# Kernel tuning notes

Measured on AMD Instinct MI355X. Metric: run time of the kernel, lower is better.

The kernel has to match this reference:

```python
import jax, jax.numpy as jnp
import numpy as np
from jax import lax

E = 3  # num_experts

def _maxpool2(x):
    return lax.reduce_window(x, -jnp.inf, lax.max, (1, 1, 2, 2), (1, 1, 2, 2), 'VALID')

def _mixed_conv(x, experts, routing, stride, pad):
    # per-sample expert-mixed convolution via grouped conv trick
    B, Ci, H, W = x.shape
    _, Co, _, k, _ = experts.shape
    kern = jnp.einsum('be,eoikl->boikl', routing, experts).reshape(B * Co, Ci, k, k)
    y = lax.conv_general_dilated(
        x.reshape(1, B * Ci, H, W), kern, (stride, stride),
        [(pad, pad), (pad, pad)],
        dimension_numbers=('NCHW', 'OIHW', 'NCHW'),
        feature_group_count=B)
    return y.reshape(B, Co, y.shape[2], y.shape[3])

def _dyres_conv(x, experts, rw, rb, stride=1, pad=1):
    # DyRes mode 'A': routing from avg-pool + spatial-std descriptors, softmax over experts
    avg = x.mean((2, 3))
    std = x.std((2, 3))
    r = jax.nn.softmax((avg + std) @ rw.T + rb, axis=-1)  # [B, E]
    return _mixed_conv(x, experts, r, stride, pad)

def _cond_conv(x, experts, rw, rb, stride=1, pad=1):
    # CondConv: sigmoid routing from global average pool
    r = jax.nn.sigmoid(x.mean((2, 3)) @ rw.T + rb)  # [B, E]
    return _mixed_conv(x, experts, r, stride, pad)

def _conv_init(key, co, ci, k):
    return jax.random.normal(key, (E, co, ci, k, k), jnp.float32) * np.sqrt(2.0 / (ci * k * k)).astype(np.float32)

def setup_inputs() -> dict:
    key = jax.random.key(0)
    ks = jax.random.split(key, 20)
    B = 512
    d = {}
    d['x'] = jax.random.normal(ks[0], (B, 3, 32, 32), jnp.float32)
    d['dw1'] = _conv_init(ks[1], 64, 3, 3)
    d['rw1'] = jax.random.normal(ks[2], (E, 3), jnp.float32) * 0.1
    d['rb1'] = jnp.zeros((E,), jnp.float32)
    d['dw2'] = _conv_init(ks[3], 192, 64, 3)
    d['rw2'] = jax.random.normal(ks[4], (E, 64), jnp.float32) * 0.1
    d['rb2'] = jnp.zeros((E,), jnp.float32)
    d['dw3'] = _conv_init(ks[5], 384, 192, 3)
    d['rw3'] = jax.random.normal(ks[6], (E, 192), jnp.float32) * 0.1
    d['rb3'] = jnp.zeros((E,), jnp.float32)
    d['cw4'] = _conv_init(ks[7], 256, 384, 3)
    d['cr4w'] = jax.random.normal(ks[8], (E, 384), jnp.float32) * 0.1
    d['cr4b'] = jnp.zeros((E,), jnp.float32)
    d['cw5'] = _conv_init(ks[9], 256, 256, 3)
    d['cr5w'] = jax.random.normal(ks[10], (E, 256), jnp.float32) * 0.1
    d['cr5b'] = jnp.zeros((E,), jnp.float32)
    d['fw1'] = jax.random.normal(ks[11], (4096, 1024), jnp.float32) * np.sqrt(2.0 / 1024).astype(np.float32)
    d['fb1'] = jnp.zeros((4096,), jnp.float32)
    d['fw2'] = jax.random.normal(ks[12], (4096, 4096), jnp.float32) * np.sqrt(2.0 / 4096).astype(np.float32)
    d['fb2'] = jnp.zeros((4096,), jnp.float32)
    d['fw3'] = jax.random.normal(ks[13], (100, 4096), jnp.float32) * np.sqrt(1.0 / 4096).astype(np.float32)
    d['fb3'] = jnp.zeros((100,), jnp.float32)
    return d

def reference(x, dw1, rw1, rb1, dw2, rw2, rb2, dw3, rw3, rb3,
              cw4, cr4w, cr4b, cw5, cr5w, cr5b,
              fw1, fb1, fw2, fb2, fw3, fb3):
    h = jax.nn.relu(_dyres_conv(x, dw1, rw1, rb1, stride=2))   # [B,64,16,16]
    h = _maxpool2(h)                                           # [B,64,8,8]
    h = jax.nn.relu(_dyres_conv(h, dw2, rw2, rb2))             # [B,192,8,8]
    h = _maxpool2(h)                                           # [B,192,4,4]
    h = jax.nn.relu(_dyres_conv(h, dw3, rw3, rb3))             # [B,384,4,4]
    h = jax.nn.relu(_cond_conv(h, cw4, cr4w, cr4b))            # [B,256,4,4]
    h = jax.nn.relu(_cond_conv(h, cw5, cr5w, cr5b))            # [B,256,4,4]
    h = _maxpool2(h)                                           # [B,256,2,2]
    h = h.reshape(h.shape[0], -1)                              # [B,1024]
    h = jax.nn.relu(h @ fw1.T + fb1)
    h = jax.nn.relu(h @ fw2.T + fb2)
    return h @ fw3.T + fb3                                     # [B,100]
```

## Files before the change

kernel.cpp:

```cpp
#include <hip/hip_runtime.h>
#include <math.h>


typedef unsigned short u16;
typedef unsigned int u32;
typedef short bf16x8 __attribute__((ext_vector_type(8)));
typedef float f32x4 __attribute__((ext_vector_type(4)));

__device__ __forceinline__ u16 bf16_rne(float f) {
    u32 u = __float_as_uint(f);
    return (u16)((u + 0x7fffu + ((u >> 16) & 1u)) >> 16);
}
__device__ __forceinline__ u32 packsplit(float v) {
    u16 h = bf16_rne(v);
    float hf = __uint_as_float((u32)h << 16);
    u16 l = bf16_rne(v - hf);
    return ((u32)h << 16) | l;
}
__device__ __forceinline__ float unpackf(u32 p) {
    return __uint_as_float(p & 0xffff0000u) + __uint_as_float(p << 16);
}
__device__ __forceinline__ int xcd_swz(int bid, int n) {
    if ((n & 7) != 0) return bid;
    int cpx = n >> 3;
    return (bid & 7) * cpx + (bid >> 3);
}

__global__ __launch_bounds__(256)
void wsplit_kernel(const float* __restrict__ W, u16* __restrict__ whi,
                   u16* __restrict__ wlo, int total, int Kper, int Kpad)
{
    int idx = blockIdx.x * 256 + threadIdx.x;
    if (idx >= total) return;
    int r = idx / Kpad, k = idx - r * Kpad;
    float v = (k < Kper) ? W[(size_t)r * Kper + k] : 0.f;
    u16 h = bf16_rne(v);
    whi[idx] = h;
    wlo[idx] = bf16_rne(v - __uint_as_float((u32)h << 16));
}

__global__ __launch_bounds__(256)
void wsplit_cl_kernel(const float* __restrict__ W, u16* __restrict__ whi,
                      u16* __restrict__ wlo, int total, int Ci)
{
    int idx = blockIdx.x * 256 + threadIdx.x;
    if (idx >= total) return;
    int Kper = 9 * Ci;
    int r = idx / Kper, kp = idx - r * Kper;
    int cell = kp / Ci, ci = kp - cell * Ci;
    float v = W[(size_t)r * Kper + ci * 9 + cell];
    u16 h = bf16_rne(v);
    whi[idx] = h;
    wlo[idx] = bf16_rne(v - __uint_as_float((u32)h << 16));
}

__global__ __launch_bounds__(64)
void stats_kernel(const float* __restrict__ actv, float* __restrict__ s,
                  int C, int HW, int use_std)
{
    int idx = blockIdx.x;
    size_t base = (size_t)idx * HW;
    int lane = threadIdx.x;
    float sum = 0.f, sq = 0.f;
    const float* p = actv + base;
    for (int i = lane; i < HW; i += 64) { float v = p[i]; sum += v; sq += v * v; }
#pragma unroll
    for (int off = 32; off > 0; off >>= 1) {
        sum += __shfl_down(sum, off);
        sq  += __shfl_down(sq, off);
    }
    if (lane == 0) {
        float inv = 1.f / (float)HW;
        float mean = sum * inv;
        float var = sq * inv - mean * mean;
        float outv = mean;
        if (use_std) outv += sqrtf(fmaxf(var, 0.f));
        s[idx] = outv;
    }
}

__global__ __launch_bounds__(384)
void stats_cl_kernel(const u32* __restrict__ act, float* __restrict__ s,
                     int H2, int W2, int C, int use_std)
{
    int b = blockIdx.x, c = threadIdx.x;
    int Hin = H2 - 2, Win = W2 - 2;
    float sum = 0.f, sq = 0.f;
    for (int h = 0; h < Hin; ++h)
        for (int w = 0; w < Win; ++w) {
            float v = unpackf(act[(((size_t)b * H2 + h + 1) * W2 + w + 1) * C + c]);
            sum += v; sq += v * v;
        }
    float inv = 1.f / (float)(Hin * Win);
    float mean = sum * inv;
    float var = sq * inv - mean * mean;
    float outv = mean;
    if (use_std) outv += sqrtf(fmaxf(var, 0.f));
    s[b * C + c] = outv;
}

__global__ __launch_bounds__(64)
void routing_kernel(const float* __restrict__ s, const float* __restrict__ rw,
                    const float* __restrict__ rb, float* __restrict__ r,
                    int C, int softmax_mode)
{
    int b = blockIdx.x;
    int lane = threadIdx.x;
    float d0 = 0.f, d1 = 0.f, d2 = 0.f;
    for (int c = lane; c < C; c += 64) {
        float sv = s[b * C + c];
        d0 += sv * rw[c];
        d1 += sv * rw[C + c];
        d2 += sv * rw[2 * C + c];
    }
#pragma unroll
    for (int off = 32; off > 0; off >>= 1) {
        d0 += __shfl_down(d0, off);
        d1 += __shfl_down(d1, off);
        d2 += __shfl_down(d2, off);
    }
    if (lane == 0) {
        d0 += rb[0]; d1 += rb[1]; d2 += rb[2];
        if (softmax_mode) {
            float mx = fmaxf(d0, fmaxf(d1, d2));
            float e0 = expf(d0 - mx), e1 = expf(d1 - mx), e2 = expf(d2 - mx);
            float inv = 1.f / (e0 + e1 + e2);
            r[b * 3 + 0] = e0 * inv;
            r[b * 3 + 1] = e1 * inv;
            r[b * 3 + 2] = e2 * inv;
        } else {
            r[b * 3 + 0] = 1.f / (1.f + expf(-d0));
            r[b * 3 + 1] = 1.f / (1.f + expf(-d1));
            r[b * 3 + 2] = 1.f / (1.f + expf(-d2));
        }
    }
}

template<int CI, int H2, int W2, int LGS, int LGOW>
__global__ __launch_bounds__(256, 2)
void cgemm_cl_kernel(const u16* __restrict__ Whi, const u16* __restrict__ Wlo,
                     const u32* __restrict__ Bpk, const float* __restrict__ rptr,
                     float* __restrict__ Cout, int M, int N, int Kper, int Kchunk)
{
    __shared__ __align__(16) u16 Ah[2][128 * 40], Al[2][128 * 40];
    __shared__ __align__(16) u16 Bh[2][128 * 40], Bl[2][128 * 40];
    const int tid = threadIdx.x;
    const int bx = xcd_swz(blockIdx.x, gridDim.x);
    const int n0 = bx << 7, m0 = blockIdx.y << 7;
    const int kq0 = blockIdx.z * Kchunk;

    const int rowA = tid >> 1, kh16 = (tid & 1) << 4;
    const int nB = tid & 127, kOff = (tid >> 7) << 4;

    const int nn = n0 + nB;
    const int bB = nn >> LGS;
    const int sidx = nn & ((1 << LGS) - 1);
    const int oh = sidx >> LGOW, ow = sidx & ((1 << LGOW) - 1);
    const long nBase = ((long)(bB * H2 + oh) * W2 + ow) * CI;

    const int lane = tid & 63, wv = tid >> 6;
    const int lm = lane & 15, qd = lane >> 4;
    const int wm = (wv & 1) << 6, wn = (wv >> 1) << 6;

    float rsv[3][4];
#pragma unroll
    for (int ni = 0; ni < 4; ++ni) {
        int n = n0 + wn + ni * 16 + lm;
        int b = n >> LGS;
#pragma unroll
        for (int e = 0; e < 3; ++e) rsv[e][ni] = rptr[b * 3 + e];
    }

    f32x4 acc[4][4], accS[4][4];
#pragma unroll
    for (int i = 0; i < 4; ++i)
#pragma unroll
        for (int j = 0; j < 4; ++j) {
            acc[i][j]  = (f32x4){0.f, 0.f, 0.f, 0.f};
            accS[i][j] = (f32x4){0.f, 0.f, 0.f, 0.f};
        }

    const int mg = m0 + rowA;
    const int nkz = Kchunk >> 5;
    const int NS = 3 * nkz;

    int eL = 0, kL = kq0;
    uint4 pA0, pA1, pA2, pA3;
    uint4 pQ0, pQ1, pQ2, pQ3;

    auto LOAD = [&]() {
        size_t aOff = ((size_t)(eL * M + mg)) * Kper + kL + kh16;
        const u16* hp = Whi + aOff;
        const u16* lp = Wlo + aOff;
        pA0 = *(const uint4*)hp; pA1 = *(const uint4*)(hp + 8);
        pA2 = *(const uint4*)lp; pA3 = *(const uint4*)(lp + 8);
        int k = kL + kOff;
        int cell = k / CI;
        int ci0 = k - cell * CI;
        int kh = (cell * 11) >> 5;
        int kw = cell - kh * 3;
        const u32* bp = Bpk + (nBase + (long)((kh * W2 + kw) * CI + ci0));
        pQ0 = *(const uint4*)bp;
        pQ1 = *(const uint4*)(bp + 4);
        pQ2 = *(const uint4*)(bp + 8);
        pQ3 = *(const uint4*)(bp + 12);
    };
    auto ADV = [&]() {
        kL += 32;
        if (kL == kq0 + Kchunk) { kL = kq0; ++eL; }
    };
    auto STORE = [&](int buf) {
        *(uint4*)(&Ah[buf][rowA * 40 + kh16])     = pA0;
        *(uint4*)(&Ah[buf][rowA * 40 + kh16 + 8]) = pA1;
        *(uint4*)(&Al[buf][rowA * 40 + kh16])     = pA2;
        *(uint4*)(&Al[buf][rowA * 40 + kh16 + 8]) = pA3;
        u32 qv[16] = {pQ0.x, pQ0.y, pQ0.z, pQ0.w, pQ1.x, pQ1.y, pQ1.z, pQ1.w,
                      pQ2.x, pQ2.y, pQ2.z, pQ2.w, pQ3.x, pQ3.y, pQ3.z, pQ3.w};
        u32 hw[8], lw[8];
#pragma unroll
        for (int j = 0; j < 8; ++j) {
            u32 p0 = qv[2 * j], p1 = qv[2 * j + 1];
            hw[j] = (p0 >> 16) | (p1 & 0xffff0000u);
            lw[j] = (p0 & 0xffffu) | (p1 << 16);
        }
        *(uint4*)(&Bh[buf][nB * 40 + kOff])     = make_uint4(hw[0], hw[1], hw[2], hw[3]);
        *(uint4*)(&Bh[buf][nB * 40 + kOff + 8]) = make_uint4(hw[4], hw[5], hw[6], hw[7]);
        *(uint4*)(&Bl[buf][nB * 40 + kOff])     = make_uint4(lw[0], lw[1], lw[2], lw[3]);
        *(uint4*)(&Bl[buf][nB * 40 + kOff + 8]) = make_uint4(lw[4], lw[5], lw[6], lw[7]);
    };
    auto COMPUTE = [&](int buf) {
        bf16x8 ah[4], al[4];
#pragma unroll
        for (int mi = 0; mi < 4; ++mi) {
            int row = wm + mi * 16 + lm;
            ah[mi] = *(const bf16x8*)(&Ah[buf][row * 40 + qd * 8]);
            al[mi] = *(const bf16x8*)(&Al[buf][row * 40 + qd * 8]);
        }
        __builtin_amdgcn_s_setprio(1);
#pragma unroll
        for (int ni = 0; ni < 4; ++ni) {
            int row = wn + ni * 16 + lm;
            bf16x8 bh = *(const bf16x8*)(&Bh[buf][row * 40 + qd * 8]);
            bf16x8 bl = *(const bf16x8*)(&Bl[buf][row * 40 + qd * 8]);
#pragma unroll
            for (int mi = 0; mi < 4; ++mi) {
                f32x4 c = acc[mi][ni];
                c = __builtin_amdgcn_mfma_f32_16x16x32_bf16(al[mi], bh, c, 0, 0, 0);
                c = __builtin_amdgcn_mfma_f32_16x16x32_bf16(ah[mi], bl, c, 0, 0, 0);
                c = __builtin_amdgcn_mfma_f32_16x16x32_bf16(ah[mi], bh, c, 0, 0, 0);
                acc[mi][ni] = c;
            }
        }
        __builtin_amdgcn_s_setprio(0);
    };

    LOAD(); ADV();
    int s = 0, buf = 0;
#pragma unroll
    for (int e = 0; e < 3; ++e) {
        for (int t = 0; t < nkz; ++t) {
            STORE(buf);
            if (s + 1 < NS) { LOAD(); ADV(); }
            asm volatile("s_waitcnt lgkmcnt(0)\n\ts_barrier" ::: "memory");
            COMPUTE(buf);
            buf ^= 1; ++s;
        }
#pragma unroll
        for (int mi = 0; mi < 4; ++mi)
#pragma unroll
            for (int ni = 0; ni < 4; ++ni) {
                accS[mi][ni] += acc[mi][ni] * rsv[e][ni];
                acc[mi][ni] = (f32x4){0.f, 0.f, 0.f, 0.f};
            }
    }

    const bool atom = (gridDim.z > 1);
#pragma unroll
    for (int ni = 0; ni < 4; ++ni) {
        int n = n0 + wn + ni * 16 + lm;
#pragma unroll
        for (int mi = 0; mi < 4; ++mi)
#pragma unroll
            for (int r = 0; r < 4; ++r) {
                int m = m0 + wm + mi * 16 + qd * 4 + r;
                if (m >= M) continue;
                float v = accS[mi][ni][r];
                if (atom) atomicAdd(&Cout[(size_t)n * M + m], v);
                else      Cout[(size_t)n * M + m] = v;
            }
    }
}

__global__ __launch_bounds__(256, 2)
void cgemm_l1_kernel(const u16* __restrict__ Whi, const u16* __restrict__ Wlo,
                     const u32* __restrict__ Bpk, const float* __restrict__ rptr,
                     float* __restrict__ Cout, int M, int N)
{
    __shared__ __align__(16) u16 Ah[2][128 * 40], Al[2][128 * 40];
    __shared__ __align__(16) u16 Bh[2][128 * 40], Bl[2][128 * 40];
    const int tid = threadIdx.x;
    const int bx = xcd_swz(blockIdx.x, gridDim.x);
    const int n0 = bx << 7;
    const int Kper = 27, Kpad = 32;
    const int H = 32, W = 32;

    const int rowA = tid >> 1, kh16 = (tid & 1) << 4;
    const int nB = tid & 127, kOff = (tid >> 7) << 4;

    const int nn = n0 + nB;
    const int bB = nn >> 8;
    const int sidx = nn & 255;
    const int ohs = (sidx >> 4) * 2 - 1;
    const int ows = (sidx & 15) * 2 - 1;
    const long nBase = (long)bB * 3072 + (long)ohs * W + ows;

    const int lane = tid & 63, wv = tid >> 6;
    const int lm = lane & 15, qd = lane >> 4;
    const int wm = (wv & 1) << 6, wn = (wv >> 1) << 6;

    float rsv[3][4];
#pragma unroll
    for (int ni = 0; ni < 4; ++ni) {
        int n = n0 + wn + ni * 16 + lm;
        int b = n >> 8;
#pragma unroll
        for (int e = 0; e < 3; ++e) rsv[e][ni] = rptr[b * 3 + e];
    }

    f32x4 acc[4][4], accS[4][4];
#pragma unroll
    for (int i = 0; i < 4; ++i)
#pragma unroll
        for (int j = 0; j < 4; ++j) {
            acc[i][j]  = (f32x4){0.f, 0.f, 0.f, 0.f};
            accS[i][j] = (f32x4){0.f, 0.f, 0.f, 0.f};
        }

    const int mg = rowA;
    int eL = 0;
    uint4 pA0, pA1, pA2, pA3;
    u32 pB[16];

    auto LOAD = [&]() {
        size_t aOff = ((size_t)(eL * M + mg)) * Kpad + kh16;
        const u16* hp = Whi + aOff;
        const u16* lp = Wlo + aOff;
        pA0 = *(const uint4*)hp; pA1 = *(const uint4*)(hp + 8);
        pA2 = *(const uint4*)lp; pA3 = *(const uint4*)(lp + 8);
#pragma unroll
        for (int j = 0; j < 16; ++j) {
            int k = kOff + j;
            int ci = (int)((unsigned)k / 9u);
            int r9 = k - ci * 9;
            int kh = (int)(((unsigned)r9 * 11u) >> 5);
            int kw = r9 - kh * 3;
            int ih = ohs + kh, iw = ows + kw;
            u32 p = 0;
            if (k < Kper && (unsigned)ih < (unsigned)H && (unsigned)iw < (unsigned)W)
                p = Bpk[nBase + (long)ci * 1024 + kh * W + kw];
            pB[j] = p;
        }
    };
    auto STORE = [&](int buf) {
        *(uint4*)(&Ah[buf][rowA * 40 + kh16])     = pA0;
        *(uint4*)(&Ah[buf][rowA * 40 + kh16 + 8]) = pA1;
        *(uint4*)(&Al[buf][rowA * 40 + kh16])     = pA2;
        *(uint4*)(&Al[buf][rowA * 40 + kh16 + 8]) = pA3;
        u32 hw[8], lw[8];
#pragma unroll
        for (int j = 0; j < 8; ++j) {
            u32 p0 = pB[2 * j], p1 = pB[2 * j + 1];
            hw[j] = (p0 >> 16) | (p1 & 0xffff0000u);
            lw[j] = (p0 & 0xffffu) | (p1 << 16);
        }
        *(uint4*)(&Bh[buf][nB * 40 + kOff])     = make_uint4(hw[0], hw[1], hw[2], hw[3]);
        *(uint4*)(&Bh[buf][nB * 40 + kOff + 8]) = make_uint4(hw[4], hw[5], hw[6], hw[7]);
        *(uint4*)(&Bl[buf][nB * 40 + kOff])     = make_uint4(lw[0], lw[1], lw[2], lw[3]);
        *(uint4*)(&Bl[buf][nB * 40 + kOff + 8]) = make_uint4(lw[4], lw[5], lw[6], lw[7]);
    };
    auto COMPUTE = [&](int buf) {
        bf16x8 ah[4], al[4];
#pragma unroll
        for (int mi = 0; mi < 4; ++mi) {
            int row = wm + mi * 16 + lm;
            ah[mi] = *(const bf16x8*)(&Ah[buf][row * 40 + qd * 8]);
            al[mi] = *(const bf16x8*)(&Al[buf][row * 40 + qd * 8]);
        }
        __builtin_amdgcn_s_setprio(1);
#pragma unroll
        for (int ni = 0; ni < 4; ++ni) {
            int row = wn + ni * 16 + lm;
            bf16x8 bh = *(const bf16x8*)(&Bh[buf][row * 40 + qd * 8]);
            bf16x8 bl = *(const bf16x8*)(&Bl[buf][row * 40 + qd * 8]);
#pragma unroll
            for (int mi = 0; mi < 4; ++mi) {
                f32x4 c = acc[mi][ni];
                c = __builtin_amdgcn_mfma_f32_16x16x32_bf16(al[mi], bh, c, 0, 0, 0);
                c = __builtin_amdgcn_mfma_f32_16x16x32_bf16(ah[mi], bl, c, 0, 0, 0);
                c = __builtin_amdgcn_mfma_f32_16x16x32_bf16(ah[mi], bh, c, 0, 0, 0);
                acc[mi][ni] = c;
            }
        }
        __builtin_amdgcn_s_setprio(0);
    };

    LOAD(); ++eL;
    int buf = 0;
#pragma unroll
    for (int e = 0; e < 3; ++e) {
        STORE(buf);
        if (e < 2) { LOAD(); ++eL; }
        asm volatile("s_waitcnt lgkmcnt(0)\n\ts_barrier" ::: "memory");
        COMPUTE(buf);
        buf ^= 1;
#pragma unroll
        for (int mi = 0; mi < 4; ++mi)
#pragma unroll
            for (int ni = 0; ni < 4; ++ni) {
                accS[mi][ni] += acc[mi][ni] * rsv[e][ni];
                acc[mi][ni] = (f32x4){0.f, 0.f, 0.f, 0.f};
            }
    }

#pragma unroll
    for (int ni = 0; ni < 4; ++ni) {
        int n = n0 + wn + ni * 16 + lm;
#pragma unroll
        for (int mi = 0; mi < 4; ++mi)
#pragma unroll
            for (int r = 0; r < 4; ++r) {
                int m = wm + mi * 16 + qd * 4 + r;
                if (m >= M) continue;
                Cout[(size_t)n * M + m] = accS[mi][ni][r];
            }
    }
}

template<int BIAS, int TROUT>
__global__ __launch_bounds__(256)
void mgemm_kernel(const u16* __restrict__ Whi, const u16* __restrict__ Wlo,
                  const u32* __restrict__ Bpk, const float* __restrict__ bias,
                  float* __restrict__ Cout,
                  int M, int N, int Kpad, int Kchunk)
{
    __shared__ __align__(16) u16 Ah[128 * 40], Al[128 * 40];
    __shared__ __align__(16) u32 Bp[128 * 36];
    const int tid = threadIdx.x;
    const int n0 = blockIdx.x << 7, m0 = blockIdx.y << 7;
    const int bz = blockIdx.z;
    const int kq0 = bz * Kchunk;

    const int rowA = tid >> 1, kh16 = (tid & 1) << 4;
    const int nB = tid & 127, kOff = (tid >> 7) << 4;

    const int lane = tid & 63, wv = tid >> 6;
    const int lm = lane & 15, qd = lane >> 4;
    const int wm = (wv & 1) << 6, wn = (wv >> 1) << 6;

    f32x4 acc[4][4];
#pragma unroll
    for (int i = 0; i < 4; ++i)
#pragma unroll
        for (int j = 0; j < 4; ++j)
            acc[i][j] = (f32x4){0.f, 0.f, 0.f, 0.f};

    for (int kq = kq0; kq < kq0 + Kchunk; kq += 32) {
        {
            int mg = m0 + rowA;
            uint4 h0 = {0,0,0,0}, h1 = {0,0,0,0}, l0 = {0,0,0,0}, l1 = {0,0,0,0};
            if (mg < M) {
                const u16* hp = Whi + (size_t)mg * Kpad + kq + kh16;
                const u16* lp = Wlo + (size_t)mg * Kpad + kq + kh16;
                h0 = *(const uint4*)hp; h1 = *(const uint4*)(hp + 8);
                l0 = *(const uint4*)lp; l1 = *(const uint4*)(lp + 8);
            }
            *(uint4*)(&Ah[rowA * 40 + kh16])     = h0;
            *(uint4*)(&Ah[rowA * 40 + kh16 + 8]) = h1;
            *(uint4*)(&Al[rowA * 40 + kh16])     = l0;
            *(uint4*)(&Al[rowA * 40 + kh16 + 8]) = l1;
        }
        {
            const u32* bp = Bpk + (size_t)(n0 + nB) * Kpad + kq + kOff;
            uint4 q0 = *(const uint4*)bp;
            uint4 q1 = *(const uint4*)(bp + 4);
            uint4 q2 = *(const uint4*)(bp + 8);
            uint4 q3 = *(const uint4*)(bp + 12);
            *(uint4*)(&Bp[nB * 36 + kOff])      = q0;
            *(uint4*)(&Bp[nB * 36 + kOff + 4])  = q1;
            *(uint4*)(&Bp[nB * 36 + kOff + 8])  = q2;
            *(uint4*)(&Bp[nB * 36 + kOff + 12]) = q3;
        }
        __syncthreads();
        {
            bf16x8 ah[4], al[4];
#pragma unroll
            for (int mi = 0; mi < 4; ++mi) {
                int row = wm + mi * 16 + lm;
                ah[mi] = *(const bf16x8*)(&Ah[row * 40 + qd * 8]);
                al[mi] = *(const bf16x8*)(&Al[row * 40 + qd * 8]);
            }
#pragma unroll
            for (int ni = 0; ni < 4; ++ni) {
                int row = wn + ni * 16 + lm;
                const u32* bp = &Bp[row * 36 + qd * 8];
                uint4 p0 = *(const uint4*)bp;
                uint4 p1 = *(const uint4*)(bp + 4);
                union { u32 w[4]; bf16x8 v; } bh, bl;
                bh.w[0] = (p0.x >> 16) | (p0.y & 0xffff0000u);
                bl.w[0] = (p0.x & 0xffffu) | (p0.y << 16);
                bh.w[1] = (p0.z >> 16) | (p0.w & 0xffff0000u);
                bl.w[1] = (p0.z & 0xffffu) | (p0.w << 16);
                bh.w[2] = (p1.x >> 16) | (p1.y & 0xffff0000u);
                bl.w[2] = (p1.x & 0xffffu) | (p1.y << 16);
                bh.w[3] = (p1.z >> 16) | (p1.w & 0xffff0000u);
                bl.w[3] = (p1.z & 0xffffu) | (p1.w << 16);
#pragma unroll
                for (int mi = 0; mi < 4; ++mi) {
                    f32x4 c = acc[mi][ni];
                    c = __builtin_amdgcn_mfma_f32_16x16x32_bf16(al[mi], bh.v, c, 0, 0, 0);
                    c = __builtin_amdgcn_mfma_f32_16x16x32_bf16(ah[mi], bl.v, c, 0, 0, 0);
                    c = __builtin_amdgcn_mfma_f32_16x16x32_bf16(ah[mi], bh.v, c, 0, 0, 0);
                    acc[mi][ni] = c;
                }
            }
        }
        __syncthreads();
    }

#pragma unroll
    for (int ni = 0; ni < 4; ++ni) {
        int n = n0 + wn + ni * 16 + lm;
        if (n >= N) continue;
#pragma unroll
        for (int mi = 0; mi < 4; ++mi)
#pragma unroll
            for (int r = 0; r < 4; ++r) {
                int m = m0 + wm + mi * 16 + qd * 4 + r;
                if (m >= M) continue;
                float v = acc[mi][ni][r];
                if (BIAS && bz == 0) v += bias[m];
                if (TROUT) atomicAdd(&Cout[(size_t)n * M + m], v);
                else       atomicAdd(&Cout[(size_t)m * N + n], v);
            }
    }
}

__global__ __launch_bounds__(256)
void pack_kernel(const float* __restrict__ in, u32* __restrict__ outp, int count)
{
    int i = blockIdx.x * 256 + threadIdx.x;
    if (i >= count) return;
    outp[i] = packsplit(in[i]);
}

__global__ __launch_bounds__(256)
void pool_pack_cl_kernel(const float* __restrict__ in, u32* __restrict__ outp,
                         int Bn, int Hin, int Win, int C)
{
    int OH = Hin >> 1, OW = Win >> 1, H2 = OH + 2, W2 = OW + 2;
    int total = Bn * H2 * W2 * C;
    int i = blockIdx.x * 256 + threadIdx.x;
    if (i >= total) return;
    int c = i % C; int t = i / C;
    int w = t % W2; t /= W2;
    int h = t % H2; int b = t / H2;
    u32 pv = 0;
    if (h >= 1 && h <= OH && w >= 1 && w <= OW) {
        int oh = h - 1, ow = w - 1;
        const float* p = in + (((size_t)b * Hin + 2 * oh) * Win + 2 * ow) * C + c;
        size_t rs = (size_t)Win * C;
        float v = fmaxf(fmaxf(p[0], p[C]), fmaxf(p[rs], p[rs + C]));
        pv = packsplit(fmaxf(v, 0.f));
    }
    outp[i] = pv;
}

__global__ __launch_bounds__(256)
void pack_cl_kernel(const float* __restrict__ in, u32* __restrict__ outp,
                    int Bn, int Hin, int Win, int C)
{
    int H2 = Hin + 2, W2 = Win + 2;
    int total = Bn * H2 * W2 * C;
    int i = blockIdx.x * 256 + threadIdx.x;
    if (i >= total) return;
    int c = i % C; int t = i / C;
    int w = t % W2; t /= W2;
    int h = t % H2; int b = t / H2;
    u32 pv = 0;
    if (h >= 1 && h <= Hin && w >= 1 && w <= Win) {
        float v = in[(((size_t)b * Hin + (h - 1)) * Win + (w - 1)) * C + c];
        pv = packsplit(fmaxf(v, 0.f));
    }
    outp[i] = pv;
}

__global__ __launch_bounds__(256)
void pool_flatten_cl_kernel(const float* __restrict__ in, u32* __restrict__ outp)
{
    int i = blockIdx.x * 256 + threadIdx.x;
    if (i >= 512 * 1024) return;
    int b = i >> 10;
    int f = i & 1023;
    int c = f >> 2, sp = f & 3;
    int oh = sp >> 1, ow = sp & 1;
    const float* p = in + (((size_t)b * 4 + 2 * oh) * 4 + 2 * ow) * 256 + c;
    float v = fmaxf(fmaxf(p[0], p[256]), fmaxf(p[1024], p[1024 + 256]));
    outp[i] = packsplit(fmaxf(v, 0.f));
}

__global__ __launch_bounds__(256)
void tp_pack_kernel(const float* __restrict__ in, u32* __restrict__ outp,
                    int Mt, int Nt)
{
    __shared__ float t[32][33];
    int tx = threadIdx.x & 31, ty = threadIdx.x >> 5;
    int mB = blockIdx.x << 5, nB = blockIdx.y << 5;
#pragma unroll
    for (int i = 0; i < 4; ++i) {
        int mm = ty + i * 8;
        t[mm][tx] = in[(size_t)(mB + mm) * Nt + nB + tx];
    }
    __syncthreads();
#pragma unroll
    for (int i = 0; i < 4; ++i) {
        int nn = ty + i * 8;
        float v = fmaxf(t[tx][nn], 0.f);
        outp[(size_t)(nB + nn) * Mt + mB + tx] = packsplit(v);
    }
}

extern "C" void kernel_launch(void* const* d_in, const int* in_sizes, int n_in,
                              void* d_out, int out_size, void* d_ws, size_t ws_size,
                              hipStream_t stream)
{
    const float* x    = (const float*)d_in[0];
    const float* dw1  = (const float*)d_in[1];
    const float* rw1  = (const float*)d_in[2];
    const float* rb1  = (const float*)d_in[3];
    const float* dw2  = (const float*)d_in[4];
    const float* rw2  = (const float*)d_in[5];
    const float* rb2  = (const float*)d_in[6];
    const float* dw3  = (const float*)d_in[7];
    const float* rw3  = (const float*)d_in[8];
    const float* rb3  = (const float*)d_in[9];
    const float* cw4  = (const float*)d_in[10];
    const float* cr4w = (const float*)d_in[11];
    const float* cr4b = (const float*)d_in[12];
    const float* cw5  = (const float*)d_in[13];
    const float* cr5w = (const float*)d_in[14];
    const float* cr5b = (const float*)d_in[15];
    const float* fw1  = (const float*)d_in[16];
    const float* fb1  = (const float*)d_in[17];
    const float* fw2  = (const float*)d_in[18];
    const float* fb2  = (const float*)d_in[19];
    const float* fw3  = (const float*)d_in[20];
    const float* fb3  = (const float*)d_in[21];
    float* out = (float*)d_out;

    float* ws    = (float*)d_ws;
    float* r1    = ws;
    float* r2    = r1 + 1536;
    float* r3    = r2 + 1536;
    float* r4    = r3 + 1536;
    float* r5    = r4 + 1536;
    float* sdesc = ws + 8192 + 65536;
    const size_t REGION = 18874368;
    float* region = sdesc + 196608;
    float* slab   = region;
    u32*   a3u    = (u32*)(region + 4194304);
    u16*   regEnd = (u16*)(region + REGION);
    u32*   P1     = (u32*)(region + REGION);

    u16 *w1h = regEnd - 2*(size_t)6144,     *w1l = regEnd - (size_t)6144;
    u16 *w2h = regEnd - 2*(size_t)331776,   *w2l = regEnd - (size_t)331776;
    u16 *w3h = regEnd - 2*(size_t)1990656,  *w3l = regEnd - (size_t)1990656;
    u16 *w4h = regEnd - 2*(size_t)2654208,  *w4l = regEnd - (size_t)2654208;
    u16 *w5h = regEnd - 2*(size_t)1769472,  *w5l = regEnd - (size_t)1769472;
    u16 *f1h = regEnd - 2*(size_t)4194304,  *f1l = regEnd - (size_t)4194304;
    u16 *f2h = regEnd - 2*(size_t)16777216, *f2l = regEnd - (size_t)16777216;
    u16 *f3h = regEnd - 2*(size_t)409600,   *f3l = regEnd - (size_t)409600;

    u32* xpk   = P1;
    u32* a1    = P1;
    u32* a2    = P1;
    u32* a4    = P1;
    u32* hTpk  = P1;
    u32* f1pkT = P1 + 1048576;
    u32* f2pkT = P1 + 3145728;

    const int B = 512;

    pack_kernel<<<6144, 256, 0, stream>>>(x, xpk, 1572864);

    wsplit_kernel<<<24, 256, 0, stream>>>(dw1, w1h, w1l, 6144, 27, 32);
    stats_kernel<<<B * 3, 64, 0, stream>>>(x, sdesc, 3, 1024, 1);
    routing_kernel<<<B, 64, 0, stream>>>(sdesc, rw1, rb1, r1, 3, 1);
    cgemm_l1_kernel<<<dim3(1024, 1, 1), 256, 0, stream>>>(
        w1h, w1l, xpk, r1, slab, 64, 131072);
    pool_pack_cl_kernel<<<12800, 256, 0, stream>>>(slab, a1, B, 16, 16, 64);

    wsplit_cl_kernel<<<1296, 256, 0, stream>>>(dw2, w2h, w2l, 331776, 64);
    stats_cl_kernel<<<B, 64, 0, stream>>>(a1, sdesc, 10, 10, 64, 1);
    routing_kernel<<<B, 64, 0, stream>>>(sdesc, rw2, rb2, r2, 64, 1);
    cgemm_cl_kernel<64, 10, 10, 6, 3><<<dim3(256, 2, 1), 256, 0, stream>>>(
        w2h, w2l, a1, r2, slab, 192, 32768, 576, 576);
    pool_pack_cl_kernel<<<13824, 256, 0, stream>>>(slab, a2, B, 8, 8, 192);

    wsplit_cl_kernel<<<7776, 256, 0, stream>>>(dw3, w3h, w3l, 1990656, 192);
    stats_cl_kernel<<<B, 192, 0, stream>>>(a2, sdesc, 6, 6, 192, 1);
    routing_kernel<<<B, 64, 0, stream>>>(sdesc, rw3, rb3, r3, 192, 1);
    hipMemsetAsync(slab, 0, (size_t)8192 * 384 * 4, stream);
    cgemm_cl_kernel<192, 6, 6, 4, 2><<<dim3(64, 3, 2), 256, 0, stream>>>(
        w3h, w3l, a2, r3, slab, 384, 8192, 1728, 864);
    pack_cl_kernel<<<27648, 256, 0, stream>>>(slab, a3u, B, 4, 4, 384);

    wsplit_cl_kernel<<<10368, 256, 0, stream>>>(cw4, w4h, w4l, 2654208, 384);
    stats_cl_kernel<<<B, 384, 0, stream>>>(a3u, sdesc, 6, 6, 384, 0);
    routing_kernel<<<B, 64, 0, stream>>>(sdesc, cr4w, cr4b, r4, 384, 0);
    hipMemsetAsync(slab, 0, (size_t)8192 * 256 * 4, stream);
    cgemm_cl_kernel<384, 6, 6, 4, 2><<<dim3(64, 2, 4), 256, 0, stream>>>(
        w4h, w4l, a3u, r4, slab, 256, 8192, 3456, 864);
    pack_cl_kernel<<<18432, 256, 0, stream>>>(slab, a4, B, 4, 4, 256);

    wsplit_cl_kernel<<<6912, 256, 0, stream>>>(cw5, w5h, w5l, 1769472, 256);
    stats_cl_kernel<<<B, 256, 0, stream>>>(a4, sdesc, 6, 6, 256, 0);
    routing_kernel<<<B, 64, 0, stream>>>(sdesc, cr5w, cr5b, r5, 256, 0);
    hipMemsetAsync(slab, 0, (size_t)8192 * 256 * 4, stream);
    cgemm_cl_kernel<256, 6, 6, 4, 2><<<dim3(64, 2, 4), 256, 0, stream>>>(
        w5h, w5l, a4, r5, slab, 256, 8192, 2304, 576);

    pool_flatten_cl_kernel<<<2048, 256, 0, stream>>>(slab, hTpk);

    wsplit_kernel<<<16384, 256, 0, stream>>>(fw1, f1h, f1l, 4194304, 1024, 1024);
    hipMemsetAsync(slab, 0, (size_t)4096 * 512 * 4, stream);
    mgemm_kernel<1, 0><<<dim3(4, 32, 8), 256, 0, stream>>>(
        f1h, f1l, hTpk, fb1, slab, 4096, 512, 1024, 128);
    tp_pack_kernel<<<dim3(128, 16), 256, 0, stream>>>(slab, f1pkT, 4096, 512);

    wsplit_kernel<<<65536, 256, 0, stream>>>(fw2, f2h, f2l, 16777216, 4096, 4096);
    hipMemsetAsync(slab, 0, (size_t)4096 * 512 * 4, stream);
    mgemm_kernel<1, 0><<<dim3(4, 32, 8), 256, 0, stream>>>(
        f2h, f2l, f1pkT, fb2, slab, 4096, 512, 4096, 512);
    tp_pack_kernel<<<dim3(128, 16), 256, 0, stream>>>(slab, f2pkT, 4096, 512);

    wsplit_kernel<<<1600, 256, 0, stream>>>(fw3, f3h, f3l, 409600, 4096, 4096);
    hipMemsetAsync(out, 0, (size_t)512 * 100 * 4, stream);
    mgemm_kernel<1, 1><<<dim3(4, 1, 32), 256, 0, stream>>>(
        f3h, f3l, f2pkT, fb3, out, 100, 512, 4096, 128);
}
```

Baseline: 1.473 ms.

## Load weight fragments directly from global memory into registers, bypassing LDS

The A (weight hi/lo) tiles are no longer staged through shared memory. Each wave now loads its MFMA fragments straight from global memory into registers, with the next step's fragments prefetched after compute. This removes the LDS writes and reads for A and halves LDS usage. In exchange each A element is loaded redundantly by the two waves that share the same rows, loads are less coalesced (16-byte per lane across strided rows), and register pressure rises, which may hurt occupancy.

```diff
diff --git a/kernel.cpp b/kernel.cpp
--- a/kernel.cpp
+++ b/kernel.cpp
@@ -142,14 +142,12 @@
                      const u32* __restrict__ Bpk, const float* __restrict__ rptr,
                      float* __restrict__ Cout, int M, int N, int Kper, int Kchunk)
 {
-    __shared__ __align__(16) u16 Ah[2][128 * 40], Al[2][128 * 40];
     __shared__ __align__(16) u16 Bh[2][128 * 40], Bl[2][128 * 40];
     const int tid = threadIdx.x;
     const int bx = xcd_swz(blockIdx.x, gridDim.x);
     const int n0 = bx << 7, m0 = blockIdx.y << 7;
     const int kq0 = blockIdx.z * Kchunk;
 
-    const int rowA = tid >> 1, kh16 = (tid & 1) << 4;
     const int nB = tid & 127, kOff = (tid >> 7) << 4;
 
     const int nn = n0 + nB;
@@ -180,20 +178,18 @@
             accS[i][j] = (f32x4){0.f, 0.f, 0.f, 0.f};
         }
 
-    const int mg = m0 + rowA;
     const int nkz = Kchunk >> 5;
     const int NS = 3 * nkz;
 
-    int eL = 0, kL = kq0;
-    uint4 pA0, pA1, pA2, pA3;
+    int kL = kq0;
     uint4 pQ0, pQ1, pQ2, pQ3;
-
-    auto LOAD = [&]() {
-        size_t aOff = ((size_t)(eL * M + mg)) * Kper + kL + kh16;
-        const u16* hp = Whi + aOff;
-        const u16* lp = Wlo + aOff;
-        pA0 = *(const uint4*)hp; pA1 = *(const uint4*)(hp + 8);
-        pA2 = *(const uint4*)lp; pA3 = *(const uint4*)(lp + 8);
+    int eA = 0, kA = kq0;
+    bf16x8 aH[4], aL[4];
+    const size_t aRowOff = ((size_t)(m0 + wm + lm)) * Kper + qd * 8;
+    const size_t aMiStep = (size_t)16 * Kper;
+    const size_t aEStep  = (size_t)M * Kper;
+
+    auto LOAD_B = [&]() {
         int k = kL + kOff;
         int cell = k / CI;
         int ci0 = k - cell * CI;
@@ -204,16 +200,19 @@
         pQ1 = *(const uint4*)(bp + 4);
         pQ2 = *(const uint4*)(bp + 8);
         pQ3 = *(const uint4*)(bp + 12);
+        kL += 32; if (kL == kq0 + Kchunk) kL = kq0;
     };
-    auto ADV = [&]() {
-        kL += 32;
-        if (kL == kq0 + Kchunk) { kL = kq0; ++eL; }
+    auto LOAD_A = [&]() {
+        const u16* hp = Whi + (size_t)eA * aEStep + aRowOff + kA;
+        const u16* lp = Wlo + (size_t)eA * aEStep + aRowOff + kA;
+#pragma unroll
+        for (int mi = 0; mi < 4; ++mi) {
+            aH[mi] = *(const bf16x8*)(hp + (size_t)mi * aMiStep);
+            aL[mi] = *(const bf16x8*)(lp + (size_t)mi * aMiStep);
+        }
+        kA += 32; if (kA == kq0 + Kchunk) { kA = kq0; ++eA; }
     };
-    auto STORE = [&](int buf) {
-        *(uint4*)(&Ah[buf][rowA * 40 + kh16])     = pA0;
-        *(uint4*)(&Ah[buf][rowA * 40 + kh16 + 8]) = pA1;
-        *(uint4*)(&Al[buf][rowA * 40 + kh16])     = pA2;
-        *(uint4*)(&Al[buf][rowA * 40 + kh16 + 8]) = pA3;
+    auto STORE_B = [&](int buf) {
         u32 qv[16] = {pQ0.x, pQ0.y, pQ0.z, pQ0.w, pQ1.x, pQ1.y, pQ1.z, pQ1.w,
                       pQ2.x, pQ2.y, pQ2.z, pQ2.w, pQ3.x, pQ3.y, pQ3.z, pQ3.w};
         u32 hw[8], lw[8];
@@ -229,13 +228,6 @@
         *(uint4*)(&Bl[buf][nB * 40 + kOff + 8]) = make_uint4(lw[4], lw[5], lw[6], lw[7]);
     };
     auto COMPUTE = [&](int buf) {
-        bf16x8 ah[4], al[4];
-#pragma unroll
-        for (int mi = 0; mi < 4; ++mi) {
-            int row = wm + mi * 16 + lm;
-            ah[mi] = *(const bf16x8*)(&Ah[buf][row * 40 + qd * 8]);
-            al[mi] = *(const bf16x8*)(&Al[buf][row * 40 + qd * 8]);
-        }
         __builtin_amdgcn_s_setprio(1);
 #pragma unroll
         for (int ni = 0; ni < 4; ++ni) {
@@ -245,24 +237,26 @@
 #pragma unroll
             for (int mi = 0; mi < 4; ++mi) {
                 f32x4 c = acc[mi][ni];
-                c = __builtin_amdgcn_mfma_f32_16x16x32_bf16(al[mi], bh, c, 0, 0, 0);
-                c = __builtin_amdgcn_mfma_f32_16x16x32_bf16(ah[mi], bl, c, 0, 0, 0);
-                c = __builtin_amdgcn_mfma_f32_16x16x32_bf16(ah[mi], bh, c, 0, 0, 0);
+                c = __builtin_amdgcn_mfma_f32_16x16x32_bf16(aL[mi], bh, c, 0, 0, 0);
+                c = __builtin_amdgcn_mfma_f32_16x16x32_bf16(aH[mi], bl, c, 0, 0, 0);
+                c = __builtin_amdgcn_mfma_f32_16x16x32_bf16(aH[mi], bh, c, 0, 0, 0);
                 acc[mi][ni] = c;
             }
         }
         __builtin_amdgcn_s_setprio(0);
     };
 
-    LOAD(); ADV();
+    LOAD_B();
+    LOAD_A();
     int s = 0, buf = 0;
 #pragma unroll
     for (int e = 0; e < 3; ++e) {
         for (int t = 0; t < nkz; ++t) {
-            STORE(buf);
-            if (s + 1 < NS) { LOAD(); ADV(); }
+            STORE_B(buf);
+            if (s + 1 < NS) LOAD_B();
             asm volatile("s_waitcnt lgkmcnt(0)\n\ts_barrier" ::: "memory");
             COMPUTE(buf);
+            if (s + 1 < NS) LOAD_A();
             buf ^= 1; ++s;
         }
 #pragma unroll
```

Result: slower. 1.714 ms (+16.3%).

## Reorder expert loop inside K loop to reuse B tile across experts

Applied to the files above, without the earlier changes.

Restructures the mixed-conv GEMM so that each 32-wide K step loads the activation (B) tile once and applies all three expert weight tiles to it, instead of looping experts outermost and reloading B three times. B is kept packed in LDS and split into hi/lo bf16 in registers after the read. The per-expert scaling becomes a telescoping accumulation with routing differences (r0-r1, r1-r2, r2), which lets acc keep accumulating across experts. This cuts B global loads and LDS stores by roughly a factor of three, but adds per-step scale-accumulate work, extra VGPR pressure from the register-held B fragments, and different floating-point rounding from the difference-based weighting.

```diff
diff --git a/kernel.cpp b/kernel.cpp
--- a/kernel.cpp
+++ b/kernel.cpp
@@ -143,7 +143,7 @@
                      float* __restrict__ Cout, int M, int N, int Kper, int Kchunk)
 {
     __shared__ __align__(16) u16 Ah[2][128 * 40], Al[2][128 * 40];
-    __shared__ __align__(16) u16 Bh[2][128 * 40], Bl[2][128 * 40];
+    __shared__ __align__(16) u32 Bp[2][128 * 36];
     const int tid = threadIdx.x;
     const int bx = xcd_swz(blockIdx.x, gridDim.x);
     const int n0 = bx << 7, m0 = blockIdx.y << 7;
@@ -162,13 +162,17 @@
     const int lm = lane & 15, qd = lane >> 4;
     const int wm = (wv & 1) << 6, wn = (wv >> 1) << 6;
 
-    float rsv[3][4];
+    float sv0[4], sv1[4], sv2[4];
 #pragma unroll
     for (int ni = 0; ni < 4; ++ni) {
         int n = n0 + wn + ni * 16 + lm;
         int b = n >> LGS;
-#pragma unroll
-        for (int e = 0; e < 3; ++e) rsv[e][ni] = rptr[b * 3 + e];
+        float r0v = rptr[b * 3 + 0];
+        float r1v = rptr[b * 3 + 1];
+        float r2v = rptr[b * 3 + 2];
+        sv0[ni] = r0v - r1v;
+        sv1[ni] = r1v - r2v;
+        sv2[ni] = r2v;
     }
 
     f32x4 acc[4][4], accS[4][4];
@@ -182,19 +186,23 @@
 
     const int mg = m0 + rowA;
     const int nkz = Kchunk >> 5;
-    const int NS = 3 * nkz;
-
-    int eL = 0, kL = kq0;
+    const int kEnd = kq0 + Kchunk;
+
     uint4 pA0, pA1, pA2, pA3;
     uint4 pQ0, pQ1, pQ2, pQ3;
-
-    auto LOAD = [&]() {
+    uint4 pBF[8];
+
+    int eL = 0, kL = kq0;
+    auto LOAD_A = [&]() {
         size_t aOff = ((size_t)(eL * M + mg)) * Kper + kL + kh16;
         const u16* hp = Whi + aOff;
         const u16* lp = Wlo + aOff;
         pA0 = *(const uint4*)hp; pA1 = *(const uint4*)(hp + 8);
         pA2 = *(const uint4*)lp; pA3 = *(const uint4*)(lp + 8);
-        int k = kL + kOff;
+        if (++eL == 3) { eL = 0; kL += 32; }
+    };
+    auto LOAD_B = [&](int kbase) {
+        int k = kbase + kOff;
         int cell = k / CI;
         int ci0 = k - cell * CI;
         int kh = (cell * 11) >> 5;
@@ -205,28 +213,26 @@
         pQ2 = *(const uint4*)(bp + 8);
         pQ3 = *(const uint4*)(bp + 12);
     };
-    auto ADV = [&]() {
-        kL += 32;
-        if (kL == kq0 + Kchunk) { kL = kq0; ++eL; }
-    };
-    auto STORE = [&](int buf) {
+    auto STORE_A = [&](int buf) {
         *(uint4*)(&Ah[buf][rowA * 40 + kh16])     = pA0;
         *(uint4*)(&Ah[buf][rowA * 40 + kh16 + 8]) = pA1;
         *(uint4*)(&Al[buf][rowA * 40 + kh16])     = pA2;
         *(uint4*)(&Al[buf][rowA * 40 + kh16 + 8]) = pA3;
-        u32 qv[16] = {pQ0.x, pQ0.y, pQ0.z, pQ0.w, pQ1.x, pQ1.y, pQ1.z, pQ1.w,
-                      pQ2.x, pQ2.y, pQ2.z, pQ2.w, pQ3.x, pQ3.y, pQ3.z, pQ3.w};
-        u32 hw[8], lw[8];
-#pragma unroll
-        for (int j = 0; j < 8; ++j) {
-            u32 p0 = qv[2 * j], p1 = qv[2 * j + 1];
-            hw[j] = (p0 >> 16) | (p1 & 0xffff0000u);
-            lw[j] = (p0 & 0xffffu) | (p1 << 16);
-        }
-        *(uint4*)(&Bh[buf][nB * 40 + kOff])     = make_uint4(hw[0], hw[1], hw[2], hw[3]);
-        *(uint4*)(&Bh[buf][nB * 40 + kOff + 8]) = make_uint4(hw[4], hw[5], hw[6], hw[7]);
-        *(uint4*)(&Bl[buf][nB * 40 + kOff])     = make_uint4(lw[0], lw[1], lw[2], lw[3]);
-        *(uint4*)(&Bl[buf][nB * 40 + kOff + 8]) = make_uint4(lw[4], lw[5], lw[6], lw[7]);
+    };
+    auto STORE_B = [&](int bb) {
+        u32* bp = &Bp[bb][nB * 36 + kOff];
+        *(uint4*)(bp)      = pQ0;
+        *(uint4*)(bp + 4)  = pQ1;
+        *(uint4*)(bp + 8)  = pQ2;
+        *(uint4*)(bp + 12) = pQ3;
+    };
+    auto READ_BF = [&](int bb) {
+#pragma unroll
+        for (int ni = 0; ni < 4; ++ni) {
+            const u32* bp = &Bp[bb][(wn + ni * 16 + lm) * 36 + qd * 8];
+            pBF[2 * ni]     = *(const uint4*)bp;
+            pBF[2 * ni + 1] = *(const uint4*)(bp + 4);
+        }
     };
     auto COMPUTE = [&](int buf) {
         bf16x8 ah[4], al[4];
@@ -239,39 +245,78 @@
         __builtin_amdgcn_s_setprio(1);
 #pragma unroll
         for (int ni = 0; ni < 4; ++ni) {
-            int row = wn + ni * 16 + lm;
-            bf16x8 bh = *(const bf16x8*)(&Bh[buf][row * 40 + qd * 8]);
-            bf16x8 bl = *(const bf16x8*)(&Bl[buf][row * 40 + qd * 8]);
+            uint4 p0 = pBF[2 * ni], p1 = pBF[2 * ni + 1];
+            union { u32 w[4]; bf16x8 v; } bh, bl;
+            bh.w[0] = (p0.x >> 16) | (p0.y & 0xffff0000u);
+            bl.w[0] = (p0.x & 0xffffu) | (p0.y << 16);
+            bh.w[1] = (p0.z >> 16) | (p0.w & 0xffff0000u);
+            bl.w[1] = (p0.z & 0xffffu) | (p0.w << 16);
+            bh.w[2] = (p1.x >> 16) | (p1.y & 0xffff0000u);
+            bl.w[2] = (p1.x & 0xffffu) | (p1.y << 16);
+            bh.w[3] = (p1.z >> 16) | (p1.w & 0xffff0000u);
+            bl.w[3] = (p1.z & 0xffffu) | (p1.w << 16);
 #pragma unroll
             for (int mi = 0; mi < 4; ++mi) {
                 f32x4 c = acc[mi][ni];
-                c = __builtin_amdgcn_mfma_f32_16x16x32_bf16(al[mi], bh, c, 0, 0, 0);
-                c = __builtin_amdgcn_mfma_f32_16x16x32_bf16(ah[mi], bl, c, 0, 0, 0);
-                c = __builtin_amdgcn_mfma_f32_16x16x32_bf16(ah[mi], bh, c, 0, 0, 0);
+                c = __builtin_amdgcn_mfma_f32_16x16x32_bf16(al[mi], bh.v, c, 0, 0, 0);
+                c = __builtin_amdgcn_mfma_f32_16x16x32_bf16(ah[mi], bl.v, c, 0, 0, 0);
+                c = __builtin_amdgcn_mfma_f32_16x16x32_bf16(ah[mi], bh.v, c, 0, 0, 0);
                 acc[mi][ni] = c;
             }
         }
         __builtin_amdgcn_s_setprio(0);
     };
 
-    LOAD(); ADV();
-    int s = 0, buf = 0;
-#pragma unroll
-    for (int e = 0; e < 3; ++e) {
-        for (int t = 0; t < nkz; ++t) {
-            STORE(buf);
-            if (s + 1 < NS) { LOAD(); ADV(); }
-            asm volatile("s_waitcnt lgkmcnt(0)\n\ts_barrier" ::: "memory");
-            COMPUTE(buf);
-            buf ^= 1; ++s;
-        }
+    LOAD_A();
+    LOAD_B(kq0);
+    int kB = kq0 + 32;
+    int buf = 0, bbuf = 0;
+
+    for (int t = 0; t < nkz; ++t) {
+        STORE_A(buf);
+        STORE_B(bbuf);
+        LOAD_A();
+        asm volatile("s_waitcnt lgkmcnt(0)\n\ts_barrier" ::: "memory");
+        READ_BF(bbuf);
+        COMPUTE(buf);
 #pragma unroll
         for (int mi = 0; mi < 4; ++mi)
 #pragma unroll
+            for (int ni = 0; ni < 4; ++ni)
+#pragma unroll
+                for (int c = 0; c < 4; ++c)
+                    accS[mi][ni][c] += acc[mi][ni][c] * sv0[ni];
+        buf ^= 1;
+
+        STORE_A(buf);
+        LOAD_A();
+        if (kB < kEnd) { LOAD_B(kB); kB += 32; }
+        asm volatile("s_waitcnt lgkmcnt(0)\n\ts_barrier" ::: "memory");
+        COMPUTE(buf);
+#pragma unroll
+        for (int mi = 0; mi < 4; ++mi)
+#pragma unroll
+            for (int ni = 0; ni < 4; ++ni)
+#pragma unroll
+                for (int c = 0; c < 4; ++c)
+                    accS[mi][ni][c] += acc[mi][ni][c] * sv1[ni];
+        buf ^= 1;
+
+        STORE_A(buf);
+        if (t + 1 < nkz) LOAD_A();
+        asm volatile("s_waitcnt lgkmcnt(0)\n\ts_barrier" ::: "memory");
+        COMPUTE(buf);
+#pragma unroll
+        for (int mi = 0; mi < 4; ++mi)
+#pragma unroll
             for (int ni = 0; ni < 4; ++ni) {
-                accS[mi][ni] += acc[mi][ni] * rsv[e][ni];
+#pragma unroll
+                for (int c = 0; c < 4; ++c)
+                    accS[mi][ni][c] += acc[mi][ni][c] * sv2[ni];
                 acc[mi][ni] = (f32x4){0.f, 0.f, 0.f, 0.f};
             }
+        buf ^= 1;
+        bbuf ^= 1;
     }
 
     const bool atom = (gridDim.z > 1);
```

Result: slower. 2.576 ms (+74.8%).

## Double-buffer LDS and prefetch next K tile in split-bf16 GEMM kernel

Applied to the files above, without the earlier changes.

Restructures the mgemm main loop so the next K tile's global loads go into registers while the current tile is computed from a second LDS buffer. This needs only one barrier per iteration instead of two, and global-load latency overlaps with the MFMA work. It also raises wave priority around the MFMA section and adds a min-blocks-per-CU hint to launch bounds. The cost is double the LDS footprint and extra prefetch registers, which may lower occupancy or cause spills.

```diff
diff --git a/kernel.cpp b/kernel.cpp
--- a/kernel.cpp
+++ b/kernel.cpp
@@ -437,18 +437,19 @@
 }
 
 template<int BIAS, int TROUT>
-__global__ __launch_bounds__(256)
+__global__ __launch_bounds__(256, 2)
 void mgemm_kernel(const u16* __restrict__ Whi, const u16* __restrict__ Wlo,
                   const u32* __restrict__ Bpk, const float* __restrict__ bias,
                   float* __restrict__ Cout,
                   int M, int N, int Kpad, int Kchunk)
 {
-    __shared__ __align__(16) u16 Ah[128 * 40], Al[128 * 40];
-    __shared__ __align__(16) u32 Bp[128 * 36];
+    __shared__ __align__(16) u16 Ah[2][128 * 40], Al[2][128 * 40];
+    __shared__ __align__(16) u32 Bp[2][128 * 36];
     const int tid = threadIdx.x;
     const int n0 = blockIdx.x << 7, m0 = blockIdx.y << 7;
     const int bz = blockIdx.z;
     const int kq0 = bz * Kchunk;
+    const int kEnd = kq0 + Kchunk;
 
     const int rowA = tid >> 1, kh16 = (tid & 1) << 4;
     const int nB = tid & 127, kOff = (tid >> 7) << 4;
@@ -464,67 +465,80 @@
         for (int j = 0; j < 4; ++j)
             acc[i][j] = (f32x4){0.f, 0.f, 0.f, 0.f};
 
-    for (int kq = kq0; kq < kq0 + Kchunk; kq += 32) {
-        {
-            int mg = m0 + rowA;
-            uint4 h0 = {0,0,0,0}, h1 = {0,0,0,0}, l0 = {0,0,0,0}, l1 = {0,0,0,0};
-            if (mg < M) {
-                const u16* hp = Whi + (size_t)mg * Kpad + kq + kh16;
-                const u16* lp = Wlo + (size_t)mg * Kpad + kq + kh16;
-                h0 = *(const uint4*)hp; h1 = *(const uint4*)(hp + 8);
-                l0 = *(const uint4*)lp; l1 = *(const uint4*)(lp + 8);
+    const int mg = m0 + rowA;
+    uint4 pA0, pA1, pA2, pA3;
+    uint4 pQ0, pQ1, pQ2, pQ3;
+
+    auto LOAD = [&](int kq) {
+        if (mg < M) {
+            const u16* hp = Whi + (size_t)mg * Kpad + kq + kh16;
+            const u16* lp = Wlo + (size_t)mg * Kpad + kq + kh16;
+            pA0 = *(const uint4*)hp; pA1 = *(const uint4*)(hp + 8);
+            pA2 = *(const uint4*)lp; pA3 = *(const uint4*)(lp + 8);
+        } else {
+            pA0 = make_uint4(0,0,0,0); pA1 = make_uint4(0,0,0,0);
+            pA2 = make_uint4(0,0,0,0); pA3 = make_uint4(0,0,0,0);
+        }
+        const u32* bp = Bpk + (size_t)(n0 + nB) * Kpad + kq + kOff;
+        pQ0 = *(const uint4*)bp;
+        pQ1 = *(const uint4*)(bp + 4);
+        pQ2 = *(const uint4*)(bp + 8);
+        pQ3 = *(const uint4*)(bp + 12);
+    };
+    auto STORE = [&](int buf) {
+        *(uint4*)(&Ah[buf][rowA * 40 + kh16])     = pA0;
+        *(uint4*)(&Ah[buf][rowA * 40 + kh16 + 8]) = pA1;
+        *(uint4*)(&Al[buf][rowA * 40 + kh16])     = pA2;
+        *(uint4*)(&Al[buf][rowA * 40 + kh16 + 8]) = pA3;
+        u32* bp = &Bp[buf][nB * 36 + kOff];
+        *(uint4*)(bp)      = pQ0;
+        *(uint4*)(bp + 4)  = pQ1;
+        *(uint4*)(bp + 8)  = pQ2;
+        *(uint4*)(bp + 12) = pQ3;
+    };
+    auto COMPUTE = [&](int buf) {
+        bf16x8 ah[4], al[4];
+#pragma unroll
+        for (int mi = 0; mi < 4; ++mi) {
+            int row = wm + mi * 16 + lm;
+            ah[mi] = *(const bf16x8*)(&Ah[buf][row * 40 + qd * 8]);
+            al[mi] = *(const bf16x8*)(&Al[buf][row * 40 + qd * 8]);
+        }
+        __builtin_amdgcn_s_setprio(1);
+#pragma unroll
+        for (int ni = 0; ni < 4; ++ni) {
+            const u32* bp = &Bp[buf][(wn + ni * 16 + lm) * 36 + qd * 8];
+            uint4 p0 = *(const uint4*)bp;
+            uint4 p1 = *(const uint4*)(bp + 4);
+            union { u32 w[4]; bf16x8 v; } bh, bl;
+            bh.w[0] = (p0.x >> 16) | (p0.y & 0xffff0000u);
+            bl.w[0] = (p0.x & 0xffffu) | (p0.y << 16);
+            bh.w[1] = (p0.z >> 16) | (p0.w & 0xffff0000u);
+            bl.w[1] = (p0.z & 0xffffu) | (p0.w << 16);
+            bh.w[2] = (p1.x >> 16) | (p1.y & 0xffff0000u);
+            bl.w[2] = (p1.x & 0xffffu) | (p1.y << 16);
+            bh.w[3] = (p1.z >> 16) | (p1.w & 0xffff0000u);
+            bl.w[3] = (p1.z & 0xffffu) | (p1.w << 16);
+#pragma unroll
+            for (int mi = 0; mi < 4; ++mi) {
+                f32x4 c = acc[mi][ni];
+                c = __builtin_amdgcn_mfma_f32_16x16x32_bf16(al[mi], bh.v, c, 0, 0, 0);
+                c = __builtin_amdgcn_mfma_f32_16x16x32_bf16(ah[mi], bl.v, c, 0, 0, 0);
+                c = __builtin_amdgcn_mfma_f32_16x16x32_bf16(ah[mi], bh.v, c, 0, 0, 0);
+                acc[mi][ni] = c;
             }
-            *(uint4*)(&Ah[rowA * 40 + kh16])     = h0;
-            *(uint4*)(&Ah[rowA * 40 + kh16 + 8]) = h1;
-            *(uint4*)(&Al[rowA * 40 + kh16])     = l0;
-            *(uint4*)(&Al[rowA * 40 + kh16 + 8]) = l1;
-        }
-        {
-            const u32* bp = Bpk + (size_t)(n0 + nB) * Kpad + kq + kOff;
-            uint4 q0 = *(const uint4*)bp;
-            uint4 q1 = *(const uint4*)(bp + 4);
-            uint4 q2 = *(const uint4*)(bp + 8);
-            uint4 q3 = *(const uint4*)(bp + 12);
-            *(uint4*)(&Bp[nB * 36 + kOff])      = q0;
-            *(uint4*)(&Bp[nB * 36 + kOff + 4])  = q1;
-            *(uint4*)(&Bp[nB * 36 + kOff + 8])  = q2;
-            *(uint4*)(&Bp[nB * 36 + kOff + 12]) = q3;
-        }
-        __syncthreads();
-        {
-            bf16x8 ah[4], al[4];
-#pragma unroll
-            for (int mi = 0; mi < 4; ++mi) {
-                int row = wm + mi * 16 + lm;
-                ah[mi] = *(const bf16x8*)(&Ah[row * 40 + qd * 8]);
-                al[mi] = *(const bf16x8*)(&Al[row * 40 + qd * 8]);
-            }
-#pragma unroll
-            for (int ni = 0; ni < 4; ++ni) {
-                int row = wn + ni * 16 + lm;
-                const u32* bp = &Bp[row * 36 + qd * 8];
-                uint4 p0 = *(const uint4*)bp;
-                uint4 p1 = *(const uint4*)(bp + 4);
-                union { u32 w[4]; bf16x8 v; } bh, bl;
-                bh.w[0] = (p0.x >> 16) | (p0.y & 0xffff0000u);
-                bl.w[0] = (p0.x & 0xffffu) | (p0.y << 16);
-                bh.w[1] = (p0.z >> 16) | (p0.w & 0xffff0000u);
-                bl.w[1] = (p0.z & 0xffffu) | (p0.w << 16);
-                bh.w[2] = (p1.x >> 16) | (p1.y & 0xffff0000u);
-                bl.w[2] = (p1.x & 0xffffu) | (p1.y << 16);
-                bh.w[3] = (p1.z >> 16) | (p1.w & 0xffff0000u);
-                bl.w[3] = (p1.z & 0xffffu) | (p1.w << 16);
-#pragma unroll
-                for (int mi = 0; mi < 4; ++mi) {
-                    f32x4 c = acc[mi][ni];
-                    c = __builtin_amdgcn_mfma_f32_16x16x32_bf16(al[mi], bh.v, c, 0, 0, 0);
-                    c = __builtin_amdgcn_mfma_f32_16x16x32_bf16(ah[mi], bl.v, c, 0, 0, 0);
-                    c = __builtin_amdgcn_mfma_f32_16x16x32_bf16(ah[mi], bh.v, c, 0, 0, 0);
-                    acc[mi][ni] = c;
-                }
-            }
-        }
-        __syncthreads();
+        }
+        __builtin_amdgcn_s_setprio(0);
+    };
+
+    LOAD(kq0);
+    int buf = 0;
+    for (int kq = kq0; kq < kEnd; kq += 32) {
+        STORE(buf);
+        if (kq + 32 < kEnd) LOAD(kq + 32);
+        asm volatile("s_waitcnt lgkmcnt(0)\n\ts_barrier" ::: "memory");
+        COMPUTE(buf);
+        buf ^= 1;
     }
 
 #pragma unroll
```

Result: no change. 1.486 ms (+0.8%).
